# Kernel tuning notes

Hardware: AMD Instinct MI355X
Metric: run time of the kernel (lower is better)

The kernel has to match this reference:

```python
import jax, jax.numpy as jnp
import numpy as np

T, B, D = 20, 1024, 2312  # time_steps, batch, 2*34*34 (NMNIST flattened)


def setup_inputs() -> dict:
    key = jax.random.key(0)
    k1, k2, k3, k4 = jax.random.split(key, 4)
    return {
        "x": jax.random.normal(k1, (T, B, D), dtype=jnp.float32),
        # ATIC per-feature parameters (torch inits these to zero; small random
        # values used here so gradients/gating are non-trivial for kernel tests)
        "ac": jax.random.normal(k2, (D,), dtype=jnp.float32) * 0.1,
        "tw": jax.random.normal(k3, (D,), dtype=jnp.float32) * 0.1,
        "ig": jax.random.normal(k4, (D,), dtype=jnp.float32) * 0.1,
        # LIF scalar parameters (torch defaults)
        "membrane_decay": jnp.asarray(0.8, dtype=jnp.float32),
        "synaptic_decay": jnp.asarray(0.75, dtype=jnp.float32),
        "threshold": jnp.asarray(0.8, dtype=jnp.float32),
    }


def _atic(xt, ac, tw, ig):
    # AdaptiveTemporalInformationCompression.forward on one timestep [B, D]
    p = jax.nn.softmax(xt, axis=-1)
    entropy = -jnp.sum(p * jnp.log(p + 1e-8), axis=-1)          # [B]
    compression_mask = jax.nn.sigmoid(ac * entropy[:, None])    # [B, D]
    compressed = xt * compression_mask * jax.nn.sigmoid(tw) * jax.nn.sigmoid(ig)
    binding_strength = jnp.mean(jnp.abs(compressed))             # scalar
    return compressed * binding_strength


def reference(x, ac, tw, ig, membrane_decay, synaptic_decay, threshold):
    # Per-timestep ATIC gating feeding a LIF current/membrane recurrence with
    # sigmoid surrogate spikes (surrogate_alpha = 1.0) and soft reset.
    def step(carry, xt):
        i, v = carry
        i = synaptic_decay * i + _atic(xt, ac, tw, ig)
        v = membrane_decay * v + i
        s = jax.nn.sigmoid(v - threshold)  # surrogate spike
        v = v - s * threshold              # soft reset toward reset_potential=0
        return (i, v), s

    init = (jnp.zeros((B, D), x.dtype), jnp.zeros((B, D), x.dtype))
    _, spikes = jax.lax.scan(step, init, x)  # [T, B, D]
    return spikes
```

## Files before the change

kernel.cpp:

```cpp
#include <hip/hip_runtime.h>

#define T_STEPS 20
#define B_SIZE  1024
#define D_SIZE  2312
#define BD      (B_SIZE * D_SIZE)
#define BLOCK   256
#define ROW_F4  (D_SIZE / 4)
#define F4_FULL 2
#define K2_LIM  (ROW_F4 - 2 * BLOCK)

#define ACC_STRIDE 32
#define ENT_OFF    1024
#define GEFF_OFF   (ENT_OFF + T_STEPS * B_SIZE)
#define WS_WORDS   (GEFF_OFF + D_SIZE)

__device__ __forceinline__ float sigmoidf_(float x) {
    return 1.0f / (1.0f + __expf(-x));
}

__device__ __forceinline__ float blockReduceMax(float v, float* s) {
    #pragma unroll
    for (int o = 32; o > 0; o >>= 1) v = fmaxf(v, __shfl_down(v, o, 64));
    const int wid = threadIdx.x >> 6;
    if ((threadIdx.x & 63) == 0) s[wid] = v;
    __syncthreads();
    float r = fmaxf(fmaxf(s[0], s[1]), fmaxf(s[2], s[3]));
    __syncthreads();
    return r;
}

__device__ __forceinline__ float blockReduceSum(float v, float* s) {
    #pragma unroll
    for (int o = 32; o > 0; o >>= 1) v += __shfl_down(v, o, 64);
    const int wid = threadIdx.x >> 6;
    if ((threadIdx.x & 63) == 0) s[wid] = v;
    __syncthreads();
    float r = (s[0] + s[1]) + (s[2] + s[3]);
    __syncthreads();
    return r;
}

__device__ __forceinline__ void blockReduceSum2(float& a, float& b, float* sa, float* sb) {
    #pragma unroll
    for (int o = 32; o > 0; o >>= 1) {
        a += __shfl_down(a, o, 64);
        b += __shfl_down(b, o, 64);
    }
    const int wid = threadIdx.x >> 6;
    if ((threadIdx.x & 63) == 0) { sa[wid] = a; sb[wid] = b; }
    __syncthreads();
    a = (sa[0] + sa[1]) + (sa[2] + sa[3]);
    b = (sb[0] + sb[1]) + (sb[2] + sb[3]);
    __syncthreads();
}

__global__ void prep_kernel(const float* __restrict__ tw, const float* __restrict__ ig,
                            float* __restrict__ ws) {
    const int i = blockIdx.x * BLOCK + threadIdx.x;
    if (i < T_STEPS * ACC_STRIDE) ws[i] = 0.0f;
    if (i < D_SIZE) ws[GEFF_OFF + i] = sigmoidf_(tw[i]) * sigmoidf_(ig[i]);
}

__global__ void __launch_bounds__(BLOCK)
phase1_entropy(const float* __restrict__ x, const float* __restrict__ ac,
               float* __restrict__ ws) {
    __shared__ float sA[4];
    __shared__ float sB[4];

    const int tb  = blockIdx.x;
    const int t   = tb >> 10;
    const int tid = threadIdx.x;
    const bool tail_ok = (tid < K2_LIM);

    const float4* xr = (const float4*)(x + (size_t)tb * D_SIZE);
    float4 xv[3];
    float m_l = -1e30f;
    #pragma unroll
    for (int k = 0; k < 3; ++k) {
        const bool ok = (k < F4_FULL) || tail_ok;
        xv[k] = ok ? xr[tid + k * BLOCK]
                   : make_float4(-1e30f, -1e30f, -1e30f, -1e30f);
        m_l = fmaxf(fmaxf(m_l, fmaxf(xv[k].x, xv[k].y)),
                    fmaxf(xv[k].z, xv[k].w));
    }
    const float m = blockReduceMax(m_l, sA);

    float Z = 0.0f, W = 0.0f;
    #pragma unroll
    for (int k = 0; k < 3; ++k) {
        const float u0 = xv[k].x - m, u1 = xv[k].y - m;
        const float u2 = xv[k].z - m, u3 = xv[k].w - m;
        const float e0 = __expf(u0), e1 = __expf(u1);
        const float e2 = __expf(u2), e3 = __expf(u3);
        Z += (e0 + e1) + (e2 + e3);
        W += (e0 * u0 + e1 * u1) + (e2 * u2 + e3 * u3);
    }
    blockReduceSum2(Z, W, sA, sB);
    const float H = __logf(Z) - W / Z;

    const float4* ac4 = (const float4*)ac;
    const float4* g4  = (const float4*)(ws + GEFF_OFF);
    float s_l = 0.0f;
    #pragma unroll
    for (int k = 0; k < 3; ++k) {
        const bool ok = (k < F4_FULL) || tail_ok;
        if (ok) {
            const int f = tid + k * BLOCK;
            const float4 a = ac4[f];
            const float4 g = g4[f];
            s_l += fabsf(xv[k].x * sigmoidf_(a.x * H) * g.x)
                 + fabsf(xv[k].y * sigmoidf_(a.y * H) * g.y)
                 + fabsf(xv[k].z * sigmoidf_(a.z * H) * g.z)
                 + fabsf(xv[k].w * sigmoidf_(a.w * H) * g.w);
        }
    }
    const float bs = blockReduceSum(s_l, sA);
    if (tid == 0) {
        atomicAdd(&ws[ACC_STRIDE * t], bs);
        ws[ENT_OFF + tb] = H;
    }
}

__global__ void __launch_bounds__(BLOCK)
phase2_lif(const float* __restrict__ x, const float* __restrict__ ac,
           const float* __restrict__ ws,
           const float* __restrict__ mdp, const float* __restrict__ sdp,
           const float* __restrict__ thp, float* __restrict__ out) {
    const int idx = blockIdx.x * BLOCK + threadIdx.x;
    const int e0  = idx * 4;
    const int b   = e0 / D_SIZE;
    const int d0  = e0 - b * D_SIZE;

    const float md = mdp[0];
    const float sd = sdp[0];
    const float th = thp[0];
    const float invBD = 1.0f / (float)BD;

    const float4 a = *(const float4*)(ac + d0);
    const float4 g = *(const float4*)(ws + GEFF_OFF + d0);

    float i0 = 0.f, i1 = 0.f, i2 = 0.f, i3 = 0.f;
    float v0 = 0.f, v1 = 0.f, v2 = 0.f, v3 = 0.f;

    for (int t = 0; t < T_STEPS; ++t) {
        const float4 xv = *(const float4*)(x + (size_t)t * BD + e0);
        const float H  = ws[ENT_OFF + t * B_SIZE + b];
        const float bs = ws[ACC_STRIDE * t] * invBD;

        const float c0 = xv.x * sigmoidf_(a.x * H) * g.x * bs;
        const float c1 = xv.y * sigmoidf_(a.y * H) * g.y * bs;
        const float c2 = xv.z * sigmoidf_(a.z * H) * g.z * bs;
        const float c3 = xv.w * sigmoidf_(a.w * H) * g.w * bs;

        i0 = sd * i0 + c0;  v0 = md * v0 + i0;
        i1 = sd * i1 + c1;  v1 = md * v1 + i1;
        i2 = sd * i2 + c2;  v2 = md * v2 + i2;
        i3 = sd * i3 + c3;  v3 = md * v3 + i3;

        const float s0 = sigmoidf_(v0 - th);
        const float s1 = sigmoidf_(v1 - th);
        const float s2 = sigmoidf_(v2 - th);
        const float s3 = sigmoidf_(v3 - th);
        v0 -= s0 * th;  v1 -= s1 * th;  v2 -= s2 * th;  v3 -= s3 * th;

        *(float4*)(out + (size_t)t * BD + e0) = make_float4(s0, s1, s2, s3);
    }
}

extern "C" void kernel_launch(void* const* d_in, const int* in_sizes, int n_in,
                              void* d_out, int out_size, void* d_ws, size_t ws_size,
                              hipStream_t stream) {
    const float* x   = (const float*)d_in[0];
    const float* ac  = (const float*)d_in[1];
    const float* tw  = (const float*)d_in[2];
    const float* ig  = (const float*)d_in[3];
    const float* mdp = (const float*)d_in[4];
    const float* sdp = (const float*)d_in[5];
    const float* thp = (const float*)d_in[6];
    float* out = (float*)d_out;
    float* ws  = (float*)d_ws;

    prep_kernel<<<10, BLOCK, 0, stream>>>(tw, ig, ws);

    phase1_entropy<<<T_STEPS * B_SIZE, BLOCK, 0, stream>>>(x, ac, ws);

    phase2_lif<<<BD / 4 / BLOCK, BLOCK, 0, stream>>>(x, ac, ws, mdp, sdp, thp, out);
}
```

Measured before the change: 386.1 us.

## Process one row per wavefront in entropy pass and use nontemporal spike stores

The entropy kernel now gives each 64-lane wavefront its own row, with four rows per block. This replaces the block-wide shared-memory reductions and their barriers with pure xor-shuffle wave reductions and cuts the number of blocks by four. Each lane now holds ten float4 values instead of three, which raises register pressure. The LIF kernel writes spikes with nontemporal stores so the output stream does less damage to the cache.

After: 381.4 us. Within noise of the previous version (-1.2%).

```diff
diff --git a/kernel.cpp b/kernel.cpp
--- a/kernel.cpp
+++ b/kernel.cpp
@@ -6,52 +6,37 @@
 #define BD      (B_SIZE * D_SIZE)
 #define BLOCK   256
 #define ROW_F4  (D_SIZE / 4)
-#define F4_FULL 2
-#define K2_LIM  (ROW_F4 - 2 * BLOCK)
+#define ROWS_PER_BLOCK 4
 
 #define ACC_STRIDE 32
 #define ENT_OFF    1024
 #define GEFF_OFF   (ENT_OFF + T_STEPS * B_SIZE)
 #define WS_WORDS   (GEFF_OFF + D_SIZE)
 
+typedef float floatx4 __attribute__((ext_vector_type(4)));
+
 __device__ __forceinline__ float sigmoidf_(float x) {
     return 1.0f / (1.0f + __expf(-x));
 }
 
-__device__ __forceinline__ float blockReduceMax(float v, float* s) {
+__device__ __forceinline__ float waveReduceMax(float v) {
     #pragma unroll
-    for (int o = 32; o > 0; o >>= 1) v = fmaxf(v, __shfl_down(v, o, 64));
-    const int wid = threadIdx.x >> 6;
-    if ((threadIdx.x & 63) == 0) s[wid] = v;
-    __syncthreads();
-    float r = fmaxf(fmaxf(s[0], s[1]), fmaxf(s[2], s[3]));
-    __syncthreads();
-    return r;
+    for (int o = 32; o > 0; o >>= 1) v = fmaxf(v, __shfl_xor(v, o, 64));
+    return v;
 }
 
-__device__ __forceinline__ float blockReduceSum(float v, float* s) {
+__device__ __forceinline__ float waveReduceSum(float v) {
     #pragma unroll
-    for (int o = 32; o > 0; o >>= 1) v += __shfl_down(v, o, 64);
-    const int wid = threadIdx.x >> 6;
-    if ((threadIdx.x & 63) == 0) s[wid] = v;
-    __syncthreads();
-    float r = (s[0] + s[1]) + (s[2] + s[3]);
-    __syncthreads();
-    return r;
+    for (int o = 32; o > 0; o >>= 1) v += __shfl_xor(v, o, 64);
+    return v;
 }
 
-__device__ __forceinline__ void blockReduceSum2(float& a, float& b, float* sa, float* sb) {
+__device__ __forceinline__ void waveReduceSum2(float& a, float& b) {
     #pragma unroll
     for (int o = 32; o > 0; o >>= 1) {
-        a += __shfl_down(a, o, 64);
-        b += __shfl_down(b, o, 64);
+        a += __shfl_xor(a, o, 64);
+        b += __shfl_xor(b, o, 64);
     }
-    const int wid = threadIdx.x >> 6;
-    if ((threadIdx.x & 63) == 0) { sa[wid] = a; sb[wid] = b; }
-    __syncthreads();
-    a = (sa[0] + sa[1]) + (sa[2] + sa[3]);
-    b = (sb[0] + sb[1]) + (sb[2] + sb[3]);
-    __syncthreads();
 }
 
 __global__ void prep_kernel(const float* __restrict__ tw, const float* __restrict__ ig,
@@ -64,30 +49,30 @@
 __global__ void __launch_bounds__(BLOCK)
 phase1_entropy(const float* __restrict__ x, const float* __restrict__ ac,
                float* __restrict__ ws) {
-    __shared__ float sA[4];
-    __shared__ float sB[4];
+    const int lane = threadIdx.x & 63;
+    const int tb   = blockIdx.x * ROWS_PER_BLOCK + (threadIdx.x >> 6);
+    const int t    = tb >> 10;
+    const bool tail = (lane < (ROW_F4 - 9 * 64));
 
-    const int tb  = blockIdx.x;
-    const int t   = tb >> 10;
-    const int tid = threadIdx.x;
-    const bool tail_ok = (tid < K2_LIM);
+    const float4* __restrict__ xr = (const float4*)(x + (size_t)tb * D_SIZE);
 
-    const float4* xr = (const float4*)(x + (size_t)tb * D_SIZE);
-    float4 xv[3];
+    float4 xv[10];
     float m_l = -1e30f;
     #pragma unroll
-    for (int k = 0; k < 3; ++k) {
-        const bool ok = (k < F4_FULL) || tail_ok;
-        xv[k] = ok ? xr[tid + k * BLOCK]
-                   : make_float4(-1e30f, -1e30f, -1e30f, -1e30f);
+    for (int k = 0; k < 9; ++k) {
+        xv[k] = xr[lane + (k << 6)];
         m_l = fmaxf(fmaxf(m_l, fmaxf(xv[k].x, xv[k].y)),
                     fmaxf(xv[k].z, xv[k].w));
     }
-    const float m = blockReduceMax(m_l, sA);
+    xv[9] = tail ? xr[576 + lane]
+                 : make_float4(-1e30f, -1e30f, -1e30f, -1e30f);
+    m_l = fmaxf(fmaxf(m_l, fmaxf(xv[9].x, xv[9].y)),
+                fmaxf(xv[9].z, xv[9].w));
+    const float m = waveReduceMax(m_l);
 
     float Z = 0.0f, W = 0.0f;
     #pragma unroll
-    for (int k = 0; k < 3; ++k) {
+    for (int k = 0; k < 10; ++k) {
         const float u0 = xv[k].x - m, u1 = xv[k].y - m;
         const float u2 = xv[k].z - m, u3 = xv[k].w - m;
         const float e0 = __expf(u0), e1 = __expf(u1);
@@ -95,28 +80,34 @@
         Z += (e0 + e1) + (e2 + e3);
         W += (e0 * u0 + e1 * u1) + (e2 * u2 + e3 * u3);
     }
-    blockReduceSum2(Z, W, sA, sB);
+    waveReduceSum2(Z, W);
     const float H = __logf(Z) - W / Z;
 
-    const float4* ac4 = (const float4*)ac;
-    const float4* g4  = (const float4*)(ws + GEFF_OFF);
+    const float4* __restrict__ ac4 = (const float4*)ac;
+    const float4* __restrict__ g4  = (const float4*)(ws + GEFF_OFF);
     float s_l = 0.0f;
     #pragma unroll
-    for (int k = 0; k < 3; ++k) {
-        const bool ok = (k < F4_FULL) || tail_ok;
-        if (ok) {
-            const int f = tid + k * BLOCK;
-            const float4 a = ac4[f];
-            const float4 g = g4[f];
-            s_l += fabsf(xv[k].x * sigmoidf_(a.x * H) * g.x)
-                 + fabsf(xv[k].y * sigmoidf_(a.y * H) * g.y)
-                 + fabsf(xv[k].z * sigmoidf_(a.z * H) * g.z)
-                 + fabsf(xv[k].w * sigmoidf_(a.w * H) * g.w);
-        }
+    for (int k = 0; k < 9; ++k) {
+        const int f = lane + (k << 6);
+        const float4 a = ac4[f];
+        const float4 g = g4[f];
+        s_l += fabsf(xv[k].x * sigmoidf_(a.x * H) * g.x)
+             + fabsf(xv[k].y * sigmoidf_(a.y * H) * g.y)
+             + fabsf(xv[k].z * sigmoidf_(a.z * H) * g.z)
+             + fabsf(xv[k].w * sigmoidf_(a.w * H) * g.w);
     }
-    const float bs = blockReduceSum(s_l, sA);
-    if (tid == 0) {
-        atomicAdd(&ws[ACC_STRIDE * t], bs);
+    if (tail) {
+        const int f = 576 + lane;
+        const float4 a = ac4[f];
+        const float4 g = g4[f];
+        s_l += fabsf(xv[9].x * sigmoidf_(a.x * H) * g.x)
+             + fabsf(xv[9].y * sigmoidf_(a.y * H) * g.y)
+             + fabsf(xv[9].z * sigmoidf_(a.z * H) * g.z)
+             + fabsf(xv[9].w * sigmoidf_(a.w * H) * g.w);
+    }
+    s_l = waveReduceSum(s_l);
+    if (lane == 0) {
+        atomicAdd(&ws[ACC_STRIDE * t], s_l);
         ws[ENT_OFF + tb] = H;
     }
 }
@@ -163,7 +154,8 @@
         const float s3 = sigmoidf_(v3 - th);
         v0 -= s0 * th;  v1 -= s1 * th;  v2 -= s2 * th;  v3 -= s3 * th;
 
-        *(float4*)(out + (size_t)t * BD + e0) = make_float4(s0, s1, s2, s3);
+        floatx4 sv = { s0, s1, s2, s3 };
+        __builtin_nontemporal_store(sv, (floatx4*)(out + (size_t)t * BD + e0));
     }
 }
 
@@ -182,7 +174,7 @@
 
     prep_kernel<<<10, BLOCK, 0, stream>>>(tw, ig, ws);
 
-    phase1_entropy<<<T_STEPS * B_SIZE, BLOCK, 0, stream>>>(x, ac, ws);
+    phase1_entropy<<<(T_STEPS * B_SIZE) / ROWS_PER_BLOCK, BLOCK, 0, stream>>>(x, ac, ws);
 
     phase2_lif<<<BD / 4 / BLOCK, BLOCK, 0, stream>>>(x, ac, ws, mdp, sdp, thp, out);
 }
```
